# Performance work log

Measured on AMD Instinct MI355X. Metric: run time of the kernel, lower is better.

The kernel has to match this reference:

```python
import jax, jax.numpy as jnp
from jax import lax
import numpy as np

LRELU_SLOPE = 0.2
DEMOD_EPS = 1e-8


def _mod_conv(x, style, weight, bias, demodulate, pad):
    """StyleGAN2 modulated conv via grouped conv (groups = batch).
    x: [B,Cin,H,W]; style: [B,Cin]; weight: [Cout,Cin,kh,kw]; bias: [Cout]."""
    B, Cin, H, W = x.shape
    Cout, _, kh, kw = weight.shape
    # per-sample modulated weight [B,Cout,Cin,kh,kw]
    wt = weight[None] * style[:, None, :, None, None]
    if demodulate:
        wt = wt / jnp.sqrt(jnp.sum(wt ** 2, axis=(2, 3, 4), keepdims=True) + DEMOD_EPS)
    out = lax.conv_general_dilated(
        x.reshape(1, B * Cin, H, W),
        wt.reshape(B * Cout, Cin, kh, kw),
        window_strides=(1, 1),
        padding=[(pad, pad), (pad, pad)],
        dimension_numbers=('NCHW', 'OIHW', 'NCHW'),
        feature_group_count=B,
    )
    return out.reshape(B, Cout, H, W) + bias[None, :, None, None]


def setup_inputs() -> dict:
    key = jax.random.key(0)
    ks = jax.random.split(key, 16)
    B, Cin, Cout, Wd, H = 4, 512, 256, 512, 64
    f32 = jnp.float32
    d = {
        'x': jax.random.normal(ks[0], (B, Cin, H, H), f32),
        'w': jax.random.normal(ks[1], (B, Wd), f32),
        # conv1: Cin->Cout 3x3
        'w1': jax.random.normal(ks[2], (Cout, Cin, 3, 3), f32) / np.float32(np.sqrt(Cin * 9)),
        'b1': jax.random.normal(ks[3], (Cout,), f32) * 0.01,
        'a1w': jax.random.normal(ks[4], (Cin, Wd), f32) / np.float32(np.sqrt(Wd)),
        'a1b': jnp.ones((Cin,), f32),
        # conv2: Cout->Cout 3x3
        'w2': jax.random.normal(ks[5], (Cout, Cout, 3, 3), f32) / np.float32(np.sqrt(Cout * 9)),
        'b2': jax.random.normal(ks[6], (Cout,), f32) * 0.01,
        'a2w': jax.random.normal(ks[7], (Cout, Wd), f32) / np.float32(np.sqrt(Wd)),
        'a2b': jnp.ones((Cout,), f32),
        # to_rgb: Cout->3 1x1, no demodulation
        'w3': jax.random.normal(ks[8], (3, Cout, 1, 1), f32) / np.float32(np.sqrt(Cout)),
        'b3': jax.random.normal(ks[9], (3,), f32) * 0.01,
        'a3w': jax.random.normal(ks[10], (Cout, Wd), f32) / np.float32(np.sqrt(Wd)),
        'a3b': jnp.ones((Cout,), f32),
    }
    return d


def reference(x, w, w1, b1, a1w, a1b, w2, b2, a2w, a2b, w3, b3, a3w, a3b):
    B, C, H, W = x.shape
    # nn.Upsample(scale_factor=2, mode='bilinear', align_corners=False) == half-pixel bilinear
    xu = jax.image.resize(x, (B, C, 2 * H, 2 * W), method='bilinear')
    s1 = w @ a1w.T + a1b                      # affine -> per-sample style [B,Cin]
    h = jax.nn.leaky_relu(_mod_conv(xu, s1, w1, b1, True, 1), LRELU_SLOPE)
    s2 = w @ a2w.T + a2b
    h = jax.nn.leaky_relu(_mod_conv(h, s2, w2, b2, True, 1), LRELU_SLOPE)
    s3 = w @ a3w.T + a3b
    rgb = jax.nn.leaky_relu(_mod_conv(h, s3, w3, b3, False, 0), LRELU_SLOPE)
    return (h, rgb)
```

## Files before the change

kernel.cpp:

```cpp
#include <hip/hip_runtime.h>
#include <stdint.h>

typedef __attribute__((ext_vector_type(8))) short bhalf8;
typedef __attribute__((ext_vector_type(4))) float fx4;

__device__ __forceinline__ unsigned short f2bf(float f) {
    unsigned u = __builtin_bit_cast(unsigned, f);
    unsigned r = (u + 0x7fffu + ((u >> 16) & 1u)) >> 16;
    return (unsigned short)r;
}
__device__ __forceinline__ float bf2f(unsigned short h) {
    unsigned u = ((unsigned)h) << 16;
    return __builtin_bit_cast(float, u);
}
__device__ __forceinline__ float lrelu(float v) { return v > 0.f ? v : 0.2f * v; }

typedef __attribute__((address_space(1))) void as1_void;
typedef __attribute__((address_space(3))) void as3_void;
__device__ __forceinline__ void gl_lds16(const void* g, void* l) {
    __builtin_amdgcn_global_load_lds((as1_void*)(void*)g, (as3_void*)l, 16, 0, 0);
}

__global__ __launch_bounds__(256) void style_kernel(
    const float* __restrict__ w,
    const float* __restrict__ a1w, const float* __restrict__ a1b,
    const float* __restrict__ a2w, const float* __restrict__ a2b,
    const float* __restrict__ a3w, const float* __restrict__ a3b,
    float* __restrict__ s1, float* __restrict__ s2, float* __restrict__ s3)
{
    int gw = blockIdx.x * 4 + (threadIdx.x >> 6);
    int lane = threadIdx.x & 63;
    int b = gw >> 10, r = gw & 1023;
    const float* arow; const float* abias; float* dst;
    if (r < 512)      { arow = a1w + (size_t)r * 512;        abias = a1b + r;       dst = s1 + b * 512 + r; }
    else if (r < 768) { int rr = r - 512; arow = a2w + (size_t)rr * 512; abias = a2b + rr; dst = s2 + b * 256 + rr; }
    else              { int rr = r - 768; arow = a3w + (size_t)rr * 512; abias = a3b + rr; dst = s3 + b * 256 + rr; }
    const float* wrow = w + b * 512;
    float acc = 0.f;
    #pragma unroll
    for (int j = 0; j < 8; ++j) {
        int c = lane + j * 64;
        acc += wrow[c] * arow[c];
    }
    #pragma unroll
    for (int off = 32; off; off >>= 1) acc += __shfl_down(acc, off, 64);
    if (lane == 0) *dst = acc + *abias;
}

__global__ __launch_bounds__(256) void demod_kernel(
    const float* __restrict__ w1, const float* __restrict__ w2,
    const float* __restrict__ s1, const float* __restrict__ s2,
    float* __restrict__ d1, float* __restrict__ d2)
{
    int blk = blockIdx.x;
    int conv = blk >> 10, b = (blk >> 8) & 3, o = blk & 255;
    int t = threadIdx.x;
    int cin = conv ? 256 : 512;
    const float* s = conv ? (s2 + b * 256) : (s1 + b * 512);
    const float* row = (conv ? w2 : w1) + (size_t)o * cin * 9;
    __shared__ float sv[512];
    for (int i = t; i < cin; i += 256) { float v = s[i]; sv[i] = v * v; }
    __syncthreads();
    float sum = 0.f;
    int n = cin * 9;
    for (int k = t; k < n; k += 256) {
        float v = row[k];
        sum += v * v * sv[k / 9];
    }
    #pragma unroll
    for (int off = 32; off; off >>= 1) sum += __shfl_down(sum, off, 64);
    __shared__ float red[4];
    if ((t & 63) == 0) red[t >> 6] = sum;
    __syncthreads();
    if (t == 0) {
        float tot = red[0] + red[1] + red[2] + red[3];
        (conv ? d2 : d1)[b * 256 + o] = rsqrtf(tot + 1e-8f);
    }
}

__global__ __launch_bounds__(256) void pack_kernel(
    const float* __restrict__ w1, const float* __restrict__ w2,
    unsigned short* __restrict__ wp1, unsigned short* __restrict__ wp2)
{
    int tid = blockIdx.x * 256 + threadIdx.x;
    const int N1 = 1179648, N2 = 589824;
    if (tid < N1) {
        int e = tid & 7, m = (tid >> 3) & 127, kh = (tid >> 10) & 3;
        int dx = (tid >> 12) % 3, ic = (tid / 12288) & 15;
        int dy = (tid / 196608) % 3, mblk = tid / 589824;
        int o = mblk * 128 + m, ci = ic * 32 + kh * 8 + e;
        wp1[tid] = f2bf(w1[((size_t)o * 512 + ci) * 9 + dy * 3 + dx]);
    } else if (tid < N1 + N2) {
        int t2 = tid - N1;
        int e = t2 & 7, m = (t2 >> 3) & 127, kh = (t2 >> 10) & 3;
        int dx = (t2 >> 12) % 3, ic = (t2 / 12288) & 7;
        int dy = (t2 / 98304) % 3, mblk = t2 / 294912;
        int o = mblk * 128 + m, ci = ic * 32 + kh * 8 + e;
        wp2[t2] = f2bf(w2[((size_t)o * 256 + ci) * 9 + dy * 3 + dx]);
    }
}

__global__ __launch_bounds__(256) void upsample_kernel(
    const float* __restrict__ x, const float* __restrict__ s1,
    unsigned short* __restrict__ xu)
{
    __shared__ float L[2][64][65];
    int bid = blockIdx.x, t = threadIdx.x;
    int yo = bid & 127, b = bid >> 7;
    int k = yo >> 1;
    int sy0, sy1; float wy0, wy1;
    if ((yo & 1) == 0) { sy0 = k > 0 ? k - 1 : 0; sy1 = k; wy0 = 0.25f; wy1 = 0.75f; }
    else               { sy0 = k; sy1 = k < 63 ? k + 1 : 63; wy0 = 0.75f; wy1 = 0.25f; }
    for (int c0 = 0; c0 < 512; c0 += 64) {
        __syncthreads();
        #pragma unroll
        for (int j = 0; j < 32; ++j) {
            int f = t + j * 256;
            int idx = f & 63, rowid = f >> 6;
            int cc = rowid & 63, which = rowid >> 6;
            int sy = which ? sy1 : sy0;
            L[which][cc][idx] = x[((size_t)(b * 512 + c0 + cc) * 64 + sy) * 64 + idx];
        }
        __syncthreads();
        #pragma unroll
        for (int j = 0; j < 16; ++j) {
            int it = t + j * 256;
            int cp = it & 31, xo = it >> 5;
            int kk = xo >> 1, sx0, sx1; float wx0, wx1;
            if ((xo & 1) == 0) { sx0 = kk > 0 ? kk - 1 : 0; sx1 = kk; wx0 = 0.25f; wx1 = 0.75f; }
            else               { sx0 = kk; sx1 = kk < 63 ? kk + 1 : 63; wx0 = 0.75f; wx1 = 0.25f; }
            int c = cp * 2;
            float A0 = wx0 * L[0][c][sx0] + wx1 * L[0][c][sx1];
            float B0 = wx0 * L[1][c][sx0] + wx1 * L[1][c][sx1];
            float A1 = wx0 * L[0][c + 1][sx0] + wx1 * L[0][c + 1][sx1];
            float B1 = wx0 * L[1][c + 1][sx0] + wx1 * L[1][c + 1][sx1];
            float v0 = (wy0 * A0 + wy1 * B0) * s1[b * 512 + c0 + c];
            float v1 = (wy0 * A1 + wy1 * B1) * s1[b * 512 + c0 + c + 1];
            unsigned pk = (unsigned)f2bf(v0) | ((unsigned)f2bf(v1) << 16);
            *(unsigned*)&xu[((size_t)(b * 128 + yo) * 128 + xo) * 512 + c0 + c] = pk;
        }
    }
}

template<int CIN, bool IS_CONV2>
__global__ __launch_bounds__(512, 4) void conv3x3_kernel(
    const unsigned short* __restrict__ inp,
    const unsigned short* __restrict__ wpack,
    const float* __restrict__ dvec,
    const float* __restrict__ bias,
    const float* __restrict__ post,
    unsigned short* __restrict__ outmod,
    float* __restrict__ outf)
{
    constexpr int NIC = CIN / 32;
    __shared__ __attribute__((aligned(16))) short Alds[3 * 4096];
    __shared__ __attribute__((aligned(16))) short Blds[4][4160];
    const int tid = threadIdx.x;
    const int lane = tid & 63;
    const int wvi = tid >> 6;
    const int bid = blockIdx.x;
    const int y0 = (bid & 63) << 1;
    const int mblk = (bid >> 6) & 1;
    const int b = bid >> 7;
    const int wm = (wvi >> 2) * 64;
    const int row = (wvi >> 1) & 1;
    const int wn = (wvi & 1) * 64;
    const int lhi = lane >> 4;
    const int llo = lane & 15;

    if (tid < 32) {
        int buf = tid >> 3, slot = ((tid >> 2) & 1) ? 129 : 0, part = tid & 3;
        *(int4*)((char*)&Blds[buf][0] + slot * 64 + part * 16) = make_int4(0, 0, 0, 0);
    }

    fx4 acc[4][4];
    #pragma unroll
    for (int mt = 0; mt < 4; ++mt)
        #pragma unroll
        for (int nt = 0; nt < 4; ++nt) acc[mt][nt] = (fx4){0.f, 0.f, 0.f, 0.f};

    for (int ic = 0; ic < NIC; ++ic) {
        {
            const int xg = tid >> 2, i8 = tid & 3;
            const int i8s = i8 ^ ((xg >> 1) & 3);
            #pragma unroll
            for (int rr = 0; rr < 4; ++rr) {
                const int yy = y0 - 1 + rr;
                char* dstB = (char*)&Blds[rr][0] + 64 + tid * 16;
                if ((unsigned)yy < 128u) {
                    gl_lds16(inp + ((size_t)(b * 128 + yy) * 128 + xg) * CIN + ic * 32 + i8s * 8, dstB);
                } else {
                    *(int4*)dstB = make_int4(0, 0, 0, 0);
                }
            }
        }
        {
            const unsigned short* asrc = wpack + ((size_t)(mblk * 3 + 0) * NIC + ic) * 12288;
            #pragma unroll
            for (int j = 0; j < 3; ++j) {
                int g = tid + j * 512;
                gl_lds16(asrc + (size_t)g * 8, (char*)Alds + g * 16);
            }
        }
        __syncthreads();
        #pragma unroll
        for (int dy = 0; dy < 3; ++dy) {
            const short* Brow = &Blds[row + dy][0];
            #pragma unroll
            for (int dx = 0; dx < 3; ++dx) {
                bhalf8 af[4], bfr[4];
                #pragma unroll
                for (int mt = 0; mt < 4; ++mt)
                    af[mt] = *(const bhalf8*)&Alds[dx * 4096 + (lhi * 128 + wm + mt * 16 + llo) * 8];
                #pragma unroll
                for (int nt = 0; nt < 4; ++nt) {
                    int s = wn + nt * 16 + llo + dx;
                    int key = ((s - 1) >> 1) & 3;
                    bfr[nt] = *(const bhalf8*)&Brow[s * 32 + ((lhi ^ key) << 3)];
                }
                #pragma unroll
                for (int mt = 0; mt < 4; ++mt)
                    #pragma unroll
                    for (int nt = 0; nt < 4; ++nt)
                        acc[mt][nt] = __builtin_amdgcn_mfma_f32_16x16x32_bf16(
                            af[mt], bfr[nt], acc[mt][nt], 0, 0, 0);
            }
            __syncthreads();
            if (dy < 2) {
                const unsigned short* asrc = wpack + ((size_t)(mblk * 3 + dy + 1) * NIC + ic) * 12288;
                #pragma unroll
                for (int j = 0; j < 3; ++j) {
                    int g = tid + j * 512;
                    gl_lds16(asrc + (size_t)g * 8, (char*)Alds + g * 16);
                }
                __syncthreads();
            }
        }
    }

    const int y = y0 + row;
    #pragma unroll
    for (int mt = 0; mt < 4; ++mt) {
        const int o0 = mblk * 128 + wm + mt * 16 + lhi * 4;
        const fx4 d4 = *(const fx4*)(dvec + b * 256 + o0);
        const fx4 bb4 = *(const fx4*)(bias + o0);
        const fx4 p4 = *(const fx4*)(post + b * 256 + o0);
        #pragma unroll
        for (int nt = 0; nt < 4; ++nt) {
            const int xo = wn + nt * 16 + llo;
            unsigned lo = 0, hi = 0;
            #pragma unroll
            for (int r = 0; r < 4; ++r) {
                float v = acc[mt][nt][r] * d4[r] + bb4[r];
                v = lrelu(v);
                if (IS_CONV2)
                    outf[(((size_t)b * 256 + o0 + r) * 128 + y) * 128 + xo] = v;
                unsigned short ub = f2bf(v * p4[r]);
                if (r < 2) lo |= (unsigned)ub << (16 * r);
                else       hi |= (unsigned)ub << (16 * (r - 2));
            }
            *(uint2*)&outmod[((size_t)(b * 128 + y) * 128 + xo) * 256 + o0] = make_uint2(lo, hi);
        }
    }
}

__global__ __launch_bounds__(256) void rgb_kernel(
    const unsigned short* __restrict__ hs3,
    const float* __restrict__ w3, const float* __restrict__ b3,
    float* __restrict__ out)
{
    __shared__ float wl[768];
    int t = threadIdx.x;
    for (int i = t; i < 768; i += 256) wl[i] = w3[i];
    __syncthreads();
    int p = blockIdx.x * 64 + (t >> 2);
    int q = t & 3;
    const unsigned short* src = hs3 + (size_t)p * 256 + q * 64;
    float a0 = 0.f, a1 = 0.f, a2 = 0.f;
    #pragma unroll
    for (int c8 = 0; c8 < 64; c8 += 8) {
        int4 pk = *(const int4*)(src + c8);
        #pragma unroll
        for (int qq = 0; qq < 4; ++qq) {
            unsigned uu = ((const unsigned*)&pk)[qq];
            float ve = bf2f((unsigned short)(uu & 0xffffu));
            float vo = bf2f((unsigned short)(uu >> 16));
            int c = q * 64 + c8 + qq * 2;
            a0 += ve * wl[c] + vo * wl[c + 1];
            a1 += ve * wl[256 + c] + vo * wl[256 + c + 1];
            a2 += ve * wl[512 + c] + vo * wl[512 + c + 1];
        }
    }
    a0 += __shfl_xor(a0, 1, 64); a0 += __shfl_xor(a0, 2, 64);
    a1 += __shfl_xor(a1, 1, 64); a1 += __shfl_xor(a1, 2, 64);
    a2 += __shfl_xor(a2, 1, 64); a2 += __shfl_xor(a2, 2, 64);
    int b = p >> 14, yx = p & 16383;
    if (q < 3) {
        float v = (q == 0) ? a0 : (q == 1) ? a1 : a2;
        out[((size_t)b * 3 + q) * 16384 + yx] = lrelu(v + b3[q]);
    }
}

extern "C" void kernel_launch(void* const* d_in, const int* in_sizes, int n_in,
                              void* d_out, int out_size, void* d_ws, size_t ws_size,
                              hipStream_t stream) {
    const float* x   = (const float*)d_in[0];
    const float* w   = (const float*)d_in[1];
    const float* w1  = (const float*)d_in[2];
    const float* b1  = (const float*)d_in[3];
    const float* a1w = (const float*)d_in[4];
    const float* a1b = (const float*)d_in[5];
    const float* w2  = (const float*)d_in[6];
    const float* b2  = (const float*)d_in[7];
    const float* a2w = (const float*)d_in[8];
    const float* a2b = (const float*)d_in[9];
    const float* w3  = (const float*)d_in[10];
    const float* b3  = (const float*)d_in[11];
    const float* a3w = (const float*)d_in[12];
    const float* a3b = (const float*)d_in[13];

    char* ws = (char*)d_ws;
    unsigned short* xu  = (unsigned short*)(ws);
    unsigned short* hs3 = (unsigned short*)(ws);
    unsigned short* t1  = (unsigned short*)(ws + 67108864);
    unsigned short* wp1 = (unsigned short*)(ws + 100663296);
    unsigned short* wp2 = (unsigned short*)(ws + 103022592);
    float* s1 = (float*)(ws + 104202240);
    float* s2 = (float*)(ws + 104210432);
    float* s3 = (float*)(ws + 104214528);
    float* d1 = (float*)(ws + 104218624);
    float* d2 = (float*)(ws + 104222720);

    float* h_out   = (float*)d_out;
    float* rgb_out = h_out + 16777216;

    style_kernel<<<1024, 256, 0, stream>>>(w, a1w, a1b, a2w, a2b, a3w, a3b, s1, s2, s3);
    demod_kernel<<<2048, 256, 0, stream>>>(w1, w2, s1, s2, d1, d2);
    pack_kernel<<<6912, 256, 0, stream>>>(w1, w2, wp1, wp2);
    upsample_kernel<<<512, 256, 0, stream>>>(x, s1, xu);
    conv3x3_kernel<512, false><<<512, 512, 0, stream>>>(xu, wp1, d1, b1, s2, t1, nullptr);
    conv3x3_kernel<256, true><<<512, 512, 0, stream>>>(t1, wp2, d2, b2, s3, hs3, h_out);
    rgb_kernel<<<1024, 256, 0, stream>>>(hs3, w3, b3, rgb_out);
}
```

Baseline: 381.0 us.

## Double-buffer conv weights, cover all output channels per block, stage fp32 stores via LDS

Each conv block now computes all 256 output channels (8 M-tiles per wave), so every input row tile is loaded once instead of twice. Weight tiles are double-buffered in LDS and the B rows are prefetched one dy step ahead, which removes the extra barrier and load stall per dy step. The fp32 h output is transposed through LDS so each store writes contiguous rows instead of scattered elements. The cost is double the accumulator registers (occupancy bound drops to 2) and half as many blocks (256 on the grid), which may leave compute units underused.

```diff
diff --git a/kernel.cpp b/kernel.cpp
--- a/kernel.cpp
+++ b/kernel.cpp
@@ -143,7 +143,7 @@
 }
 
 template<int CIN, bool IS_CONV2>
-__global__ __launch_bounds__(512, 4) void conv3x3_kernel(
+__global__ __launch_bounds__(512, 2) void conv3x3_kernel(
     const unsigned short* __restrict__ inp,
     const unsigned short* __restrict__ wpack,
     const float* __restrict__ dvec,
@@ -153,65 +153,83 @@
     float* __restrict__ outf)
 {
     constexpr int NIC = CIN / 32;
-    __shared__ __attribute__((aligned(16))) short Alds[3 * 4096];
+    __shared__ __attribute__((aligned(16))) short Alds[2][2][12288];
     __shared__ __attribute__((aligned(16))) short Blds[4][4160];
     const int tid = threadIdx.x;
     const int lane = tid & 63;
     const int wvi = tid >> 6;
+    const int oh = wvi >> 2;
+    const int row = (wvi >> 1) & 1;
+    const int wn = (wvi & 1) * 64;
     const int bid = blockIdx.x;
     const int y0 = (bid & 63) << 1;
-    const int mblk = (bid >> 6) & 1;
-    const int b = bid >> 7;
-    const int wm = (wvi >> 2) * 64;
-    const int row = (wvi >> 1) & 1;
-    const int wn = (wvi & 1) * 64;
+    const int b = bid >> 6;
     const int lhi = lane >> 4;
     const int llo = lane & 15;
 
+    auto stageA = [&](int bufp, int ic, int dy) {
+        const unsigned short* s0 = wpack + ((size_t)(0 + dy) * NIC + ic) * 12288;
+        const unsigned short* s1 = wpack + ((size_t)(3 + dy) * NIC + ic) * 12288;
+        #pragma unroll
+        for (int j = 0; j < 3; ++j) {
+            int g = tid + j * 512;
+            gl_lds16(s0 + (size_t)g * 8, (char*)&Alds[bufp][0][0] + g * 16);
+        }
+        #pragma unroll
+        for (int j = 0; j < 3; ++j) {
+            int g = tid + j * 512;
+            gl_lds16(s1 + (size_t)g * 8, (char*)&Alds[bufp][1][0] + g * 16);
+        }
+    };
+    auto stageB = [&](int r, int ic) {
+        int yy = y0 - 1 + r;
+        char* dst = (char*)&Blds[r][0] + 64 + tid * 16;
+        int xg = tid >> 2, i8 = tid & 3;
+        int i8s = i8 ^ ((xg >> 1) & 3);
+        if ((unsigned)yy < 128u)
+            gl_lds16(inp + ((size_t)(b * 128 + yy) * 128 + xg) * CIN + ic * 32 + i8s * 8, dst);
+        else
+            *(int4*)dst = make_int4(0, 0, 0, 0);
+    };
+
     if (tid < 32) {
-        int buf = tid >> 3, slot = ((tid >> 2) & 1) ? 129 : 0, part = tid & 3;
-        *(int4*)((char*)&Blds[buf][0] + slot * 64 + part * 16) = make_int4(0, 0, 0, 0);
-    }
-
-    fx4 acc[4][4];
-    #pragma unroll
-    for (int mt = 0; mt < 4; ++mt)
+        int r = tid >> 3, sl = (tid >> 2) & 1, part = tid & 3;
+        *(int4*)((char*)&Blds[r][0] + (sl ? 8256 : 0) + part * 16) = make_int4(0, 0, 0, 0);
+    }
+
+    fx4 acc[8][4];
+    #pragma unroll
+    for (int mt = 0; mt < 8; ++mt)
         #pragma unroll
         for (int nt = 0; nt < 4; ++nt) acc[mt][nt] = (fx4){0.f, 0.f, 0.f, 0.f};
 
+    stageA(0, 0, 0);
+    stageB(0, 0);
+    stageB(1, 0);
+    __syncthreads();
+
+    int buf = 0;
     for (int ic = 0; ic < NIC; ++ic) {
-        {
-            const int xg = tid >> 2, i8 = tid & 3;
-            const int i8s = i8 ^ ((xg >> 1) & 3);
-            #pragma unroll
-            for (int rr = 0; rr < 4; ++rr) {
-                const int yy = y0 - 1 + rr;
-                char* dstB = (char*)&Blds[rr][0] + 64 + tid * 16;
-                if ((unsigned)yy < 128u) {
-                    gl_lds16(inp + ((size_t)(b * 128 + yy) * 128 + xg) * CIN + ic * 32 + i8s * 8, dstB);
-                } else {
-                    *(int4*)dstB = make_int4(0, 0, 0, 0);
-                }
-            }
-        }
-        {
-            const unsigned short* asrc = wpack + ((size_t)(mblk * 3 + 0) * NIC + ic) * 12288;
-            #pragma unroll
-            for (int j = 0; j < 3; ++j) {
-                int g = tid + j * 512;
-                gl_lds16(asrc + (size_t)g * 8, (char*)Alds + g * 16);
-            }
-        }
-        __syncthreads();
         #pragma unroll
         for (int dy = 0; dy < 3; ++dy) {
+            if (dy == 0) {
+                stageA(buf ^ 1, ic, 1);
+                stageB(2, ic);
+            } else if (dy == 1) {
+                stageA(buf ^ 1, ic, 2);
+                stageB(3, ic);
+                if (ic + 1 < NIC) stageB(0, ic + 1);
+            } else {
+                if (ic + 1 < NIC) { stageA(buf ^ 1, ic + 1, 0); stageB(1, ic + 1); }
+            }
+            const short* Abase = &Alds[buf][oh][0];
             const short* Brow = &Blds[row + dy][0];
             #pragma unroll
             for (int dx = 0; dx < 3; ++dx) {
-                bhalf8 af[4], bfr[4];
+                bhalf8 af[8], bfr[4];
                 #pragma unroll
-                for (int mt = 0; mt < 4; ++mt)
-                    af[mt] = *(const bhalf8*)&Alds[dx * 4096 + (lhi * 128 + wm + mt * 16 + llo) * 8];
+                for (int mt = 0; mt < 8; ++mt)
+                    af[mt] = *(const bhalf8*)&Abase[dx * 4096 + (lhi * 128 + mt * 16 + llo) * 8];
                 #pragma unroll
                 for (int nt = 0; nt < 4; ++nt) {
                     int s = wn + nt * 16 + llo + dx;
@@ -219,29 +237,21 @@
                     bfr[nt] = *(const bhalf8*)&Brow[s * 32 + ((lhi ^ key) << 3)];
                 }
                 #pragma unroll
-                for (int mt = 0; mt < 4; ++mt)
+                for (int mt = 0; mt < 8; ++mt)
                     #pragma unroll
                     for (int nt = 0; nt < 4; ++nt)
                         acc[mt][nt] = __builtin_amdgcn_mfma_f32_16x16x32_bf16(
                             af[mt], bfr[nt], acc[mt][nt], 0, 0, 0);
             }
             __syncthreads();
-            if (dy < 2) {
-                const unsigned short* asrc = wpack + ((size_t)(mblk * 3 + dy + 1) * NIC + ic) * 12288;
-                #pragma unroll
-                for (int j = 0; j < 3; ++j) {
-                    int g = tid + j * 512;
-                    gl_lds16(asrc + (size_t)g * 8, (char*)Alds + g * 16);
-                }
-                __syncthreads();
-            }
+            buf ^= 1;
         }
     }
 
     const int y = y0 + row;
     #pragma unroll
-    for (int mt = 0; mt < 4; ++mt) {
-        const int o0 = mblk * 128 + wm + mt * 16 + lhi * 4;
+    for (int mt = 0; mt < 8; ++mt) {
+        const int o0 = oh * 128 + mt * 16 + lhi * 4;
         const fx4 d4 = *(const fx4*)(dvec + b * 256 + o0);
         const fx4 bb4 = *(const fx4*)(bias + o0);
         const fx4 p4 = *(const fx4*)(post + b * 256 + o0);
@@ -253,13 +263,45 @@
             for (int r = 0; r < 4; ++r) {
                 float v = acc[mt][nt][r] * d4[r] + bb4[r];
                 v = lrelu(v);
-                if (IS_CONV2)
-                    outf[(((size_t)b * 256 + o0 + r) * 128 + y) * 128 + xo] = v;
                 unsigned short ub = f2bf(v * p4[r]);
                 if (r < 2) lo |= (unsigned)ub << (16 * r);
                 else       hi |= (unsigned)ub << (16 * (r - 2));
             }
             *(uint2*)&outmod[((size_t)(b * 128 + y) * 128 + xo) * 256 + o0] = make_uint2(lo, hi);
+        }
+    }
+
+    if (IS_CONV2) {
+        float* Ef = (float*)&Alds[0][0][0];
+        #pragma unroll
+        for (int ch = 0; ch < 4; ++ch) {
+            const int rc = ch >> 1, ohc = ch & 1;
+            __syncthreads();
+            if (row == rc && oh == ohc) {
+                #pragma unroll
+                for (int mt = 0; mt < 8; ++mt) {
+                    const int o0 = ohc * 128 + mt * 16 + lhi * 4;
+                    const fx4 d4 = *(const fx4*)(dvec + b * 256 + o0);
+                    const fx4 bb4 = *(const fx4*)(bias + o0);
+                    #pragma unroll
+                    for (int nt = 0; nt < 4; ++nt) {
+                        const int xo = wn + nt * 16 + llo;
+                        #pragma unroll
+                        for (int r = 0; r < 4; ++r) {
+                            float v = lrelu(acc[mt][nt][r] * d4[r] + bb4[r]);
+                            Ef[(mt * 16 + lhi * 4 + r) * 132 + xo] = v;
+                        }
+                    }
+                }
+            }
+            __syncthreads();
+            #pragma unroll
+            for (int k = 0; k < 8; ++k) {
+                int f = k * 8192 + tid * 16;
+                int o_loc = f >> 9, off = f & 511;
+                float4 val = *(const float4*)((const char*)Ef + o_loc * 528 + off);
+                *(float4*)&outf[(((size_t)b * 256 + ohc * 128 + o_loc) * 128 + (y0 + rc)) * 128 + (off >> 2)] = val;
+            }
         }
     }
 }
@@ -338,7 +380,7 @@
     demod_kernel<<<2048, 256, 0, stream>>>(w1, w2, s1, s2, d1, d2);
     pack_kernel<<<6912, 256, 0, stream>>>(w1, w2, wp1, wp2);
     upsample_kernel<<<512, 256, 0, stream>>>(x, s1, xu);
-    conv3x3_kernel<512, false><<<512, 512, 0, stream>>>(xu, wp1, d1, b1, s2, t1, nullptr);
-    conv3x3_kernel<256, true><<<512, 512, 0, stream>>>(t1, wp2, d2, b2, s3, hs3, h_out);
+    conv3x3_kernel<512, false><<<256, 512, 0, stream>>>(xu, wp1, d1, b1, s2, t1, nullptr);
+    conv3x3_kernel<256, true><<<256, 512, 0, stream>>>(t1, wp2, d2, b2, s3, hs3, h_out);
     rgb_kernel<<<1024, 256, 0, stream>>>(hs3, w3, b3, rgb_out);
 }
```

Result: slower. 392.5 us (+3.0%).
